# Kernel optimization log

Hardware: AMD Instinct MI355X
Metric: run time of the kernel (lower is better)

The kernel has to match this reference:

```python
import jax, jax.numpy as jnp
import numpy as np

H, W = 1080, 1920
MAX_POINTS = 2048
MIN_DEPTH, MAX_DEPTH = 0.1, 2.0
# module sets intrinsics to None (bug); use realistic 1080p pinhole intrinsics
FX = 1050.0
FY = 1050.0
CX = W / 2.0
CY = H / 2.0


def setup_inputs() -> dict:
    key = jax.random.key(0)
    k1, k2 = jax.random.split(key)
    # depth in [0.2, 1.8] m so every pixel passes the validity filter
    depth_image = 0.2 + 1.6 * jax.random.uniform(k1, (H, W), dtype=jnp.float32)
    rgb_image = 255.0 * jax.random.uniform(k2, (H, W, 3), dtype=jnp.float32)
    return {"depth_image": depth_image, "rgb_image": rgb_image}


def _fps_indices(xyz, m):
    """Iterative furthest point sampling. xyz: [N,3] -> [m] int32 indices."""
    N = xyz.shape[0]
    first = jnp.array(0, dtype=jnp.int32)
    init_dists = jnp.full((N,), jnp.inf, dtype=jnp.float32)

    def body(carry, _):
        dists, last = carry
        p = xyz[last]                                 # [3]
        d = jnp.sum((xyz - p) ** 2, axis=1)           # [N]
        dists = jnp.minimum(dists, d)
        nxt = jnp.argmax(dists).astype(jnp.int32)
        return (dists, nxt), nxt

    _, rest = jax.lax.scan(body, (init_dists, first), None, length=m - 1)
    return jnp.concatenate([first[None], rest])


def reference(depth_image, rgb_image):
    # depth -> xyz  [H*W, 3]
    u, v = jnp.meshgrid(jnp.arange(W), jnp.arange(H), indexing='xy')
    u = u.reshape(-1).astype(jnp.float32)
    v = v.reshape(-1).astype(jnp.float32)
    depth = depth_image.reshape(-1)
    xyz = jnp.stack([(u - CX) * depth / FX,
                     (v - CY) * depth / FY,
                     depth], axis=1)                  # [N, 3]
    rgb = rgb_image.reshape(-1, 3) / 255.0            # [N, 3]

    # validity filter (invalid -> inf xyz, 0 rgb), as in the source
    valid = ((depth > MIN_DEPTH) & (depth < MAX_DEPTH)
             & (depth > 0) & jnp.isfinite(depth))
    vm = valid[:, None]
    valid_xyz = jnp.where(vm, xyz, jnp.inf)
    valid_rgb = jnp.where(vm, rgb, 0.0)

    # FPS sampling (N >= max_points branch)
    idx = _fps_indices(valid_xyz.astype(jnp.float32), MAX_POINTS)  # [M]
    sampled_xyz = valid_xyz[idx]                      # [M, 3]
    sampled_rgb = valid_rgb[idx]                      # [M, 3]

    # coordinate normalization to [0,1]
    xyz_min = jnp.min(sampled_xyz, axis=0, keepdims=True)
    centered = sampled_xyz - xyz_min
    xyz_max = jnp.max(centered, axis=0, keepdims=True)
    xyz_max = jnp.where(xyz_max < 1e-8, 1.0, xyz_max)
    XYZ = centered / xyz_max

    return jnp.concatenate([sampled_xyz, sampled_rgb, XYZ], axis=1)  # [M, 9]
```

## Files before the change

kernel.cpp:

```cpp
#include <hip/hip_runtime.h>
#include <math.h>

#define HH   1080
#define WW   1920
#define NPIX (HH*WW)
#define MAXP 2048
#define NTHR 512
#define NWAVE (NTHR/64)
#define PPB  8192
#define KPT  16
#define NBLK 254

#define CXF 960.0f
#define CYF 540.0f
#define FXF 1050.0f
#define FYF 1050.0f

__device__ unsigned long long g_packed[MAXP * NBLK];
__device__ unsigned long long g_win[MAXP];

__device__ __forceinline__ float proj_x(float u, float d) {
    return __fdiv_rn(__fmul_rn(__fsub_rn(u, CXF), d), FXF);
}
__device__ __forceinline__ float proj_y(float v, float d) {
    return __fdiv_rn(__fmul_rn(__fsub_rn(v, CYF), d), FYF);
}
__device__ __forceinline__ unsigned long long umax64(unsigned long long a, unsigned long long b) {
    return a > b ? a : b;
}

__global__ void zero_ws_kernel() {
    unsigned i = blockIdx.x * 256u + threadIdx.x;
    if (i < (unsigned)(MAXP * NBLK)) g_packed[i] = 0ull;
    if (i < (unsigned)MAXP)          g_win[i]    = 0ull;
}

#define FOR16(M)  M(0) M(1) M(2) M(3) M(4) M(5) M(6) M(7) M(8) M(9) M(10) M(11) M(12) M(13) M(14) M(15)
#define FOR16D(M) M(15) M(14) M(13) M(12) M(11) M(10) M(9) M(8) M(7) M(6) M(5) M(4) M(3) M(2) M(1) M(0)
#define DECLD(j) float D##j;

#define UPDJ(j) { \
    unsigned o = tid + j##u * (unsigned)NTHR; \
    float4 P = sP[o]; \
    float dx = __fsub_rn(P.x, px); \
    float dy = __fsub_rn(P.y, py); \
    float dz = __fsub_rn(P.z, pz); \
    float s  = __fadd_rn(__fadd_rn(__fmul_rn(dx, dx), __fmul_rn(dy, dy)), __fmul_rn(dz, dz)); \
    float nd = fminf(D##j, s); \
    D##j = nd; \
    if (nd >= bestd) { bestd = nd; besti = base + o; } }

__global__ __attribute__((amdgpu_flat_work_group_size(NTHR, NTHR)))
void fps_kernel(const float* __restrict__ depth, const float* __restrict__ rgb,
                float* __restrict__ out)
{
    const unsigned tid  = threadIdx.x;
    const unsigned lane = threadIdx.x & 63u;
    const unsigned wid  = threadIdx.x >> 6;
    const unsigned blk  = blockIdx.x;
    const float FINF = __int_as_float(0x7f800000);

    __shared__ float4 sP[PPB];
    __shared__ unsigned long long s_pp[NWAVE];
    __shared__ unsigned long long s_win;
    __shared__ unsigned           s_widx[MAXP];

    if (blk == (unsigned)NBLK) {
        if (wid == 0) {
            if (lane == 0) s_widx[0] = 0u;
            const bool has3 = (lane + 192u) < (unsigned)NBLK;
            for (int it = 1; it < MAXP; ++it) {
                const unsigned long long* row = &g_packed[(size_t)it * NBLK];
                unsigned long long v0, v1, v2, v3 = 0ull;
                for (;;) {
                    v0 = __hip_atomic_load(row + lane,        __ATOMIC_RELAXED, __HIP_MEMORY_SCOPE_AGENT);
                    v1 = __hip_atomic_load(row + lane + 64u,  __ATOMIC_RELAXED, __HIP_MEMORY_SCOPE_AGENT);
                    v2 = __hip_atomic_load(row + lane + 128u, __ATOMIC_RELAXED, __HIP_MEMORY_SCOPE_AGENT);
                    if (has3)
                        v3 = __hip_atomic_load(row + lane + 192u, __ATOMIC_RELAXED, __HIP_MEMORY_SCOPE_AGENT);
                    if (v0 != 0ull && v1 != 0ull && v2 != 0ull && (!has3 || v3 != 0ull)) break;
                    __builtin_amdgcn_s_sleep(1);
                }
                unsigned long long w = umax64(umax64(v0, v1), umax64(v2, v3));
                #pragma unroll
                for (int off = 32; off; off >>= 1) w = umax64(w, __shfl_xor(w, off));
                unsigned widx = 0x1FFFFFu - (unsigned)(w & 0x1FFFFFull);
                if (lane == 0) {
                    float wd = depth[widx];
                    s_widx[it] = widx;
                    __hip_atomic_store(&g_win[it],
                        ((unsigned long long)__float_as_uint(wd) << 21) |
                        (unsigned long long)(0x1FFFFFu - widx),
                        __ATOMIC_RELAXED, __HIP_MEMORY_SCOPE_AGENT);
                }
            }
        }
        __syncthreads();

        float ex[4], ey[4], ez[4], er[4], eg[4], eb[4];
        #pragma unroll
        for (int q = 0; q < 4; ++q) {
            int i = (int)tid + q * NTHR;
            unsigned sidx = s_widx[i];
            float d = depth[sidx];
            float u = (float)(sidx % WW);
            float v = (float)(sidx / WW);
            bool val = (d > 0.1f) && (d < 2.0f) && __builtin_isfinite(d);
            ex[q] = val ? proj_x(u, d) : FINF;
            ey[q] = val ? proj_y(v, d) : FINF;
            ez[q] = val ? d : FINF;
            er[q] = val ? __fdiv_rn(rgb[3u * sidx + 0u], 255.0f) : 0.0f;
            eg[q] = val ? __fdiv_rn(rgb[3u * sidx + 1u], 255.0f) : 0.0f;
            eb[q] = val ? __fdiv_rn(rgb[3u * sidx + 2u], 255.0f) : 0.0f;
        }
        float mn[3], mx[3];
        mn[0] = fminf(fminf(ex[0], ex[1]), fminf(ex[2], ex[3]));
        mx[0] = fmaxf(fmaxf(ex[0], ex[1]), fmaxf(ex[2], ex[3]));
        mn[1] = fminf(fminf(ey[0], ey[1]), fminf(ey[2], ey[3]));
        mx[1] = fmaxf(fmaxf(ey[0], ey[1]), fmaxf(ey[2], ey[3]));
        mn[2] = fminf(fminf(ez[0], ez[1]), fminf(ez[2], ez[3]));
        mx[2] = fmaxf(fmaxf(ez[0], ez[1]), fmaxf(ez[2], ez[3]));
        #pragma unroll
        for (int c = 0; c < 3; ++c) {
            for (int off = 32; off > 0; off >>= 1) {
                mn[c] = fminf(mn[c], __shfl_xor(mn[c], off));
                mx[c] = fmaxf(mx[c], __shfl_xor(mx[c], off));
            }
        }
        __shared__ float s_mn[NWAVE][3], s_mx[NWAVE][3];
        __shared__ float f_mn[3], f_sc[3];
        if (lane == 0) {
            for (int c = 0; c < 3; ++c) { s_mn[wid][c] = mn[c]; s_mx[wid][c] = mx[c]; }
        }
        __syncthreads();
        if (wid == 0) {
            float a[3], b[3];
            for (int c = 0; c < 3; ++c) {
                a[c] = (lane < NWAVE) ? s_mn[lane][c] : FINF;
                b[c] = (lane < NWAVE) ? s_mx[lane][c] : -FINF;
            }
            for (int off = NWAVE / 2; off > 0; off >>= 1) {
                for (int c = 0; c < 3; ++c) {
                    a[c] = fminf(a[c], __shfl_xor(a[c], off));
                    b[c] = fmaxf(b[c], __shfl_xor(b[c], off));
                }
            }
            if (lane == 0) {
                for (int c = 0; c < 3; ++c) {
                    f_mn[c] = a[c];
                    float m = __fsub_rn(b[c], a[c]);
                    f_sc[c] = (m < 1e-8f) ? 1.0f : m;
                }
            }
        }
        __syncthreads();
        float MN0 = f_mn[0], MN1 = f_mn[1], MN2 = f_mn[2];
        float SC0 = f_sc[0], SC1 = f_sc[1], SC2 = f_sc[2];
        #pragma unroll
        for (int q = 0; q < 4; ++q) {
            int i = (int)tid + q * NTHR;
            out[9 * i + 0] = ex[q];
            out[9 * i + 1] = ey[q];
            out[9 * i + 2] = ez[q];
            out[9 * i + 3] = er[q];
            out[9 * i + 4] = eg[q];
            out[9 * i + 5] = eb[q];
            out[9 * i + 6] = __fdiv_rn(__fsub_rn(ex[q], MN0), SC0);
            out[9 * i + 7] = __fdiv_rn(__fsub_rn(ey[q], MN1), SC1);
            out[9 * i + 8] = __fdiv_rn(__fsub_rn(ez[q], MN2), SC2);
        }
        return;
    }

    const unsigned base = blk << 13;

    FOR16(DECLD)

    #define INITJ(j) { \
        unsigned o   = tid + j##u * (unsigned)NTHR; \
        unsigned idx = base + o; \
        float x, y, z; \
        if (idx < NPIX) { \
            float d = depth[idx]; \
            float u = (float)(idx % WW); \
            float v = (float)(idx / WW); \
            bool val = (d > 0.1f) && (d < 2.0f) && __builtin_isfinite(d); \
            x = val ? proj_x(u, d) : FINF; \
            y = val ? proj_y(v, d) : FINF; \
            z = val ? d : FINF; \
            D##j = FINF; \
        } else { x = 0.f; y = 0.f; z = 0.f; D##j = -1.0f; } \
        sP[o] = make_float4(x, y, z, 0.0f); }
    FOR16(INITJ)
    __syncthreads();

    float px, py, pz;
    {
        float d = depth[0];
        bool val = (d > 0.1f) && (d < 2.0f) && __builtin_isfinite(d);
        px = val ? proj_x(0.0f, d) : FINF;
        py = val ? proj_y(0.0f, d) : FINF;
        pz = val ? d : FINF;
    }

    for (int it = 1; it < MAXP; ++it) {
        float bestd = -2.0f;
        unsigned besti = 0u;
        FOR16D(UPDJ)

        unsigned long long pk =
            ((unsigned long long)__float_as_uint(bestd) << 21) |
            (unsigned long long)(0x1FFFFFu - besti);

        #pragma unroll
        for (int off = 32; off; off >>= 1) pk = umax64(pk, __shfl_xor(pk, off));
        if (lane == 0) s_pp[wid] = pk;
        __syncthreads();

        if (wid == 0 && lane == 0) {
            unsigned long long p2 = s_pp[0];
            #pragma unroll
            for (int k = 1; k < NWAVE; ++k) p2 = umax64(p2, s_pp[k]);
            __hip_atomic_store(&g_packed[(size_t)it * NBLK + blk], p2,
                               __ATOMIC_RELAXED, __HIP_MEMORY_SCOPE_AGENT);
        }

        if (it == MAXP - 1) break;

        if (wid == 0 && lane == 0) {
            unsigned long long gv;
            for (;;) {
                gv = __hip_atomic_load(&g_win[it], __ATOMIC_RELAXED, __HIP_MEMORY_SCOPE_AGENT);
                if (gv != 0ull) break;
            }
            s_win = gv;
        }
        __syncthreads();

        unsigned long long gv = s_win;
        unsigned widx = 0x1FFFFFu - (unsigned)(gv & 0x1FFFFFull);
        float    wd   = __uint_as_float((unsigned)(gv >> 21));

        float uu = (float)(widx % WW);
        float vv = (float)(widx / WW);
        bool val = (wd > 0.1f) && (wd < 2.0f) && __builtin_isfinite(wd);
        px = val ? proj_x(uu, wd) : FINF;
        py = val ? proj_y(vv, wd) : FINF;
        pz = val ? wd : FINF;
    }
}

extern "C" void kernel_launch(void* const* d_in, const int* in_sizes, int n_in,
                              void* d_out, int out_size, void* d_ws, size_t ws_size,
                              hipStream_t stream) {
    const float* depth = (const float*)d_in[0];
    const float* rgb   = (const float*)d_in[1];
    float* out = (float*)d_out;

    zero_ws_kernel<<<dim3((MAXP * NBLK + 255) / 256), dim3(256), 0, stream>>>();

    void* args[] = { (void*)&depth, (void*)&rgb, (void*)&out };
    hipLaunchCooperativeKernel((const void*)fps_kernel, dim3(NBLK + 1), dim3(NTHR),
                               args, 0, stream);
}
```

Measured before the change: 6.762 ms.

## Use iteration-tagged double-buffered slots and LDS spin instead of per-iteration barrier

The per-iteration global rows for block partial maxima and winners are replaced by two alternating slots. Each slot is stamped with the iteration number in its top bits, so readers wait for the current tag instead of a nonzero value, and the workspace zeroing kernel shrinks to one small block. The second __syncthreads per FPS iteration is replaced by waves spinning on an LDS word, which removes one workgroup barrier from the critical path of every iteration. The cost is more complex tag-based handshaking, which depends on the existing barrier ordering to avoid slot reuse races.

After: 6.493 ms (median of 2 runs). 1.04x faster.

```diff
diff --git a/kernel.cpp b/kernel.cpp
--- a/kernel.cpp
+++ b/kernel.cpp
@@ -16,8 +16,8 @@
 #define FXF 1050.0f
 #define FYF 1050.0f
 
-__device__ unsigned long long g_packed[MAXP * NBLK];
-__device__ unsigned long long g_win[MAXP];
+__device__ unsigned long long g_packed[2 * NBLK];
+__device__ unsigned long long g_win[2];
 
 __device__ __forceinline__ float proj_x(float u, float d) {
     return __fdiv_rn(__fmul_rn(__fsub_rn(u, CXF), d), FXF);
@@ -30,9 +30,9 @@
 }
 
 __global__ void zero_ws_kernel() {
-    unsigned i = blockIdx.x * 256u + threadIdx.x;
-    if (i < (unsigned)(MAXP * NBLK)) g_packed[i] = 0ull;
-    if (i < (unsigned)MAXP)          g_win[i]    = 0ull;
+    unsigned i = threadIdx.x;
+    if (i < 2u * NBLK) g_packed[i] = 0ull;
+    if (i < 2u)        g_win[i]    = 0ull;
 }
 
 #define FOR16(M)  M(0) M(1) M(2) M(3) M(4) M(5) M(6) M(7) M(8) M(9) M(10) M(11) M(12) M(13) M(14) M(15)
@@ -70,7 +70,8 @@
             if (lane == 0) s_widx[0] = 0u;
             const bool has3 = (lane + 192u) < (unsigned)NBLK;
             for (int it = 1; it < MAXP; ++it) {
-                const unsigned long long* row = &g_packed[(size_t)it * NBLK];
+                const unsigned long long tag = (unsigned long long)it;
+                const unsigned long long* row = &g_packed[(size_t)(it & 1) * NBLK];
                 unsigned long long v0, v1, v2, v3 = 0ull;
                 for (;;) {
                     v0 = __hip_atomic_load(row + lane,        __ATOMIC_RELAXED, __HIP_MEMORY_SCOPE_AGENT);
@@ -78,7 +79,8 @@
                     v2 = __hip_atomic_load(row + lane + 128u, __ATOMIC_RELAXED, __HIP_MEMORY_SCOPE_AGENT);
                     if (has3)
                         v3 = __hip_atomic_load(row + lane + 192u, __ATOMIC_RELAXED, __HIP_MEMORY_SCOPE_AGENT);
-                    if (v0 != 0ull && v1 != 0ull && v2 != 0ull && (!has3 || v3 != 0ull)) break;
+                    if ((v0 >> 53) == tag && (v1 >> 53) == tag && (v2 >> 53) == tag &&
+                        (!has3 || (v3 >> 53) == tag)) break;
                     __builtin_amdgcn_s_sleep(1);
                 }
                 unsigned long long w = umax64(umax64(v0, v1), umax64(v2, v3));
@@ -88,7 +90,8 @@
                 if (lane == 0) {
                     float wd = depth[widx];
                     s_widx[it] = widx;
-                    __hip_atomic_store(&g_win[it],
+                    __hip_atomic_store(&g_win[it & 1],
+                        (tag << 53) |
                         ((unsigned long long)__float_as_uint(wd) << 21) |
                         (unsigned long long)(0x1FFFFFu - widx),
                         __ATOMIC_RELAXED, __HIP_MEMORY_SCOPE_AGENT);
@@ -192,6 +195,7 @@
         } else { x = 0.f; y = 0.f; z = 0.f; D##j = -1.0f; } \
         sP[o] = make_float4(x, y, z, 0.0f); }
     FOR16(INITJ)
+    if (tid == 0) s_win = 0ull;
     __syncthreads();
 
     float px, py, pz;
@@ -204,11 +208,14 @@
     }
 
     for (int it = 1; it < MAXP; ++it) {
+        const unsigned long long tag = (unsigned long long)it;
+
         float bestd = -2.0f;
         unsigned besti = 0u;
         FOR16D(UPDJ)
 
         unsigned long long pk =
+            (tag << 53) |
             ((unsigned long long)__float_as_uint(bestd) << 21) |
             (unsigned long long)(0x1FFFFFu - besti);
 
@@ -221,7 +228,7 @@
             unsigned long long p2 = s_pp[0];
             #pragma unroll
             for (int k = 1; k < NWAVE; ++k) p2 = umax64(p2, s_pp[k]);
-            __hip_atomic_store(&g_packed[(size_t)it * NBLK + blk], p2,
+            __hip_atomic_store(&g_packed[(size_t)(it & 1) * NBLK + blk], p2,
                                __ATOMIC_RELAXED, __HIP_MEMORY_SCOPE_AGENT);
         }
 
@@ -230,16 +237,19 @@
         if (wid == 0 && lane == 0) {
             unsigned long long gv;
             for (;;) {
-                gv = __hip_atomic_load(&g_win[it], __ATOMIC_RELAXED, __HIP_MEMORY_SCOPE_AGENT);
-                if (gv != 0ull) break;
-            }
-            s_win = gv;
-        }
-        __syncthreads();
-
-        unsigned long long gv = s_win;
+                gv = __hip_atomic_load(&g_win[it & 1], __ATOMIC_RELAXED, __HIP_MEMORY_SCOPE_AGENT);
+                if ((gv >> 53) == tag) break;
+            }
+            __hip_atomic_store(&s_win, gv, __ATOMIC_RELAXED, __HIP_MEMORY_SCOPE_WORKGROUP);
+        }
+        unsigned long long gv;
+        for (;;) {
+            gv = __hip_atomic_load(&s_win, __ATOMIC_RELAXED, __HIP_MEMORY_SCOPE_WORKGROUP);
+            if ((gv >> 53) == tag) break;
+        }
+
         unsigned widx = 0x1FFFFFu - (unsigned)(gv & 0x1FFFFFull);
-        float    wd   = __uint_as_float((unsigned)(gv >> 21));
+        float    wd   = __uint_as_float((unsigned)((gv >> 21) & 0xFFFFFFFFull));
 
         float uu = (float)(widx % WW);
         float vv = (float)(widx / WW);
@@ -257,7 +267,7 @@
     const float* rgb   = (const float*)d_in[1];
     float* out = (float*)d_out;
 
-    zero_ws_kernel<<<dim3((MAXP * NBLK + 255) / 256), dim3(256), 0, stream>>>();
+    zero_ws_kernel<<<dim3(1), dim3(512), 0, stream>>>();
 
     void* args[] = { (void*)&depth, (void*)&rgb, (void*)&out };
     hipLaunchCooperativeKernel((const void*)fps_kernel, dim3(NBLK + 1), dim3(NTHR),
```
